# Optimization experiments

Hardware: AMD Instinct MI355X
Metric: run time of the kernel (lower is better)

## Reference

```python
import jax, jax.numpy as jnp
import numpy as np

N, B, CIN, HID, D, K = 2048, 16, 2, 64, 16, 2


def setup_inputs() -> dict:
    key = jax.random.key(0)
    ks = jax.random.split(key, 7)
    return {
        "X": jax.random.normal(ks[0], (B, N, CIN), dtype=jnp.float32),
        "state": jax.random.normal(ks[1], (B, N, HID), dtype=jnp.float32),
        "E": jax.random.normal(ks[2], (N, D), dtype=jnp.float32),
        "gate_W": jax.random.normal(ks[3], (D, K, CIN + HID, 2 * HID), dtype=jnp.float32) * 0.1,
        "gate_b": jax.random.normal(ks[4], (D, 2 * HID), dtype=jnp.float32) * 0.1,
        "upd_W": jax.random.normal(ks[5], (D, K, CIN + HID, HID), dtype=jnp.float32) * 0.1,
        "upd_b": jax.random.normal(ks[6], (D, HID), dtype=jnp.float32) * 0.1,
    }


def avwgcn(X, E, Wp, bp, k):
    # Adaptive adjacency: softmax(relu(E E^T)) over rows, [N,N]
    n = E.shape[0]
    supports = jax.nn.softmax(jax.nn.relu(E @ E.T), axis=1)
    support_set = [jnp.eye(n, dtype=supports.dtype), supports]
    for _ in range(2, k):  # Chebyshev recursion (no-op for K=2)
        support_set.append(2.0 * supports @ support_set[-1] - support_set[-2])
    S = jnp.stack(support_set, axis=0)                      # [K,N,N]
    W = jnp.einsum('nd,dkio->nkio', E, Wp)                  # per-node weights
    bias = E @ bp                                           # [N,Co]
    Xg = jnp.einsum('knm,bmc->bknc', S, X)                  # graph conv
    Xg = Xg.transpose(0, 2, 1, 3)                           # [B,N,K,Ci]
    return jnp.einsum('bnki,nkio->bno', Xg, W) + bias


def reference(X, state, E, gate_W, gate_b, upd_W, upd_b):
    input_and_state = jnp.concatenate((X, state), axis=-1)
    z_r = jax.nn.sigmoid(avwgcn(input_and_state, E, gate_W, gate_b, K))
    z, r = z_r[..., :HID], z_r[..., HID:]
    candidate = jnp.concatenate((X, z * state), axis=-1)
    hc = jnp.tanh(avwgcn(candidate, E, upd_W, upd_b, K))
    h = r * state + (1.0 - r) * hc
    return h
```

## Files before the change

### kernel.cpp

```cpp
#include <hip/hip_runtime.h>
#include <math.h>

#define NN   2048
#define BB   16
#define CINC 2
#define HID  64
#define C1   66
#define NC   1056
#define NCP  1152
#define KI   132
#define KIP  168

typedef unsigned short u16;
typedef __attribute__((ext_vector_type(8))) short bf16x8;
typedef __attribute__((ext_vector_type(4))) float f32x4;

__device__ __forceinline__ u16 f2bf(float f) {
    union { float f; unsigned int u; } v; v.f = f;
    unsigned int r = (v.u + 0x7FFFu + ((v.u >> 16) & 1u)) >> 16;
    return (u16)r;
}
__device__ __forceinline__ float bf2f(u16 h) {
    union { unsigned int u; float f; } v; v.u = ((unsigned int)h) << 16;
    return v.f;
}

__global__ __launch_bounds__(256) void support_softmax(const float* __restrict__ E,
                                                       u16* __restrict__ S)
{
    const int n = blockIdx.x, t = threadIdx.x;
    __shared__ float red[4];
    float en[16];
#pragma unroll
    for (int d = 0; d < 16; ++d) en[d] = E[n * 16 + d];

    float v[8]; float mx = 0.f;
#pragma unroll
    for (int j = 0; j < 8; ++j) {
        const int m = t + j * 256;
        const float4* ep = (const float4*)&E[m * 16];
        float4 e0 = ep[0], e1 = ep[1], e2 = ep[2], e3 = ep[3];
        float dot = en[0]*e0.x + en[1]*e0.y + en[2]*e0.z + en[3]*e0.w
                  + en[4]*e1.x + en[5]*e1.y + en[6]*e1.z + en[7]*e1.w
                  + en[8]*e2.x + en[9]*e2.y + en[10]*e2.z + en[11]*e2.w
                  + en[12]*e3.x + en[13]*e3.y + en[14]*e3.z + en[15]*e3.w;
        dot = fmaxf(dot, 0.f);
        v[j] = dot; mx = fmaxf(mx, dot);
    }
#pragma unroll
    for (int off = 32; off; off >>= 1) mx = fmaxf(mx, __shfl_down(mx, off, 64));
    const int wid = t >> 6, lane = t & 63;
    if (lane == 0) red[wid] = mx;
    __syncthreads();
    mx = fmaxf(fmaxf(red[0], red[1]), fmaxf(red[2], red[3]));

    float s = 0.f;
#pragma unroll
    for (int j = 0; j < 8; ++j) { v[j] = expf(v[j] - mx); s += v[j]; }
#pragma unroll
    for (int off = 32; off; off >>= 1) s += __shfl_down(s, off, 64);
    __syncthreads();
    if (lane == 0) red[wid] = s;
    __syncthreads();
    s = red[0] + red[1] + red[2] + red[3];
    const float inv = 1.f / s;
#pragma unroll
    for (int j = 0; j < 8; ++j) S[n * NN + t + j * 256] = f2bf(v[j] * inv);
}

__global__ __launch_bounds__(256) void build_xcatT(const float* __restrict__ X,
                                                   const float* __restrict__ state,
                                                   u16* __restrict__ XT)
{
    const int idx = blockIdx.x * 256 + threadIdx.x;
    const int m = idx & (NN - 1), j = idx >> 11;
    float val = 0.f;
    if (j < NC) {
        const int b = j / C1, c = j - b * C1;
        val = (c < CINC) ? X[(b * NN + m) * CINC + c]
                         : state[(b * NN + m) * HID + (c - CINC)];
    }
    XT[(size_t)j * NN + m] = f2bf(val);
}

template<int O>
__global__ __launch_bounds__(256) void bias_build(const float* __restrict__ E,
                                                  const float* __restrict__ bvec,
                                                  float* __restrict__ bias)
{
    const int idx = blockIdx.x * 256 + threadIdx.x;
    const int o = idx % O, n = idx / O;
    float s = 0.f;
#pragma unroll
    for (int d = 0; d < 16; ++d) s += E[n * 16 + d] * bvec[d * O + o];
    bias[idx] = s;
}

template<int O>
__global__ __launch_bounds__(256) void wbuild(const float* __restrict__ E,
                                              const float* __restrict__ Wp,
                                              u16* __restrict__ Wall)
{
    const int t = threadIdx.x;
    const int n0 = blockIdx.y * 16;
    __shared__ float El[256];
    El[t] = E[n0 * 16 + t];
    __syncthreads();

    const int nchunks = (KI * O) / 256;
    for (int ch = blockIdx.x; ch < nchunks; ch += gridDim.x) {
        const int flat = ch * 256 + t;
        float w[16];
#pragma unroll
        for (int d = 0; d < 16; ++d) w[d] = Wp[d * (KI * O) + flat];
#pragma unroll 4
        for (int g = 0; g < 16; ++g) {
            float s = 0.f;
#pragma unroll
            for (int d = 0; d < 16; ++d) s += El[g * 16 + d] * w[d];
            Wall[(size_t)(n0 + g) * (KI * O) + flat] = f2bf(s);
        }
    }
}

__global__ __launch_bounds__(256) void gemm64(const u16* __restrict__ A,
                                              const u16* __restrict__ BT,
                                              u16* __restrict__ C)
{
    __shared__ u16 As[64 * 32];
    __shared__ u16 Bs[64 * 32];
    const int t = threadIdx.x, w = t >> 6, l = t & 63;
    const int m0 = blockIdx.y * 64, n0 = blockIdx.x * 64;
    const int wm = (w >> 1) * 32, wn = (w & 1) * 32;

    const int srow = w * 16 + (l >> 2), scol = (l & 3) * 8;
    const size_t ga0 = (size_t)(m0 + srow) * NN + scol;
    const size_t gb0 = (size_t)(n0 + srow) * NN + scol;
    const int soff = srow * 32 + scol;

    f32x4 acc[2][2];
#pragma unroll
    for (int i = 0; i < 2; ++i)
#pragma unroll
        for (int j = 0; j < 2; ++j) acc[i][j] = f32x4{0.f, 0.f, 0.f, 0.f};

    for (int k0 = 0; k0 < NN; k0 += 32) {
        bf16x8 av = *(const bf16x8*)&A[ga0 + k0];
        bf16x8 bv = *(const bf16x8*)&BT[gb0 + k0];
        *(bf16x8*)&As[soff] = av;
        *(bf16x8*)&Bs[soff] = bv;
        __syncthreads();
        bf16x8 af[2], bfr[2];
#pragma unroll
        for (int mi = 0; mi < 2; ++mi)
            af[mi] = *(const bf16x8*)&As[(wm + mi * 16 + (l & 15)) * 32 + (l >> 4) * 8];
#pragma unroll
        for (int nj = 0; nj < 2; ++nj)
            bfr[nj] = *(const bf16x8*)&Bs[(wn + nj * 16 + (l & 15)) * 32 + (l >> 4) * 8];
#pragma unroll
        for (int mi = 0; mi < 2; ++mi)
#pragma unroll
            for (int nj = 0; nj < 2; ++nj)
                acc[mi][nj] = __builtin_amdgcn_mfma_f32_16x16x32_bf16(af[mi], bfr[nj], acc[mi][nj], 0, 0, 0);
        __syncthreads();
    }
#pragma unroll
    for (int mi = 0; mi < 2; ++mi)
#pragma unroll
        for (int nj = 0; nj < 2; ++nj)
#pragma unroll
            for (int q = 0; q < 4; ++q) {
                const int row = m0 + wm + mi * 16 + (l >> 4) * 4 + q;
                const int col = n0 + wn + nj * 16 + (l & 15);
                C[(size_t)row * NCP + col] = f2bf(acc[mi][nj][q]);
            }
}

__global__ __launch_bounds__(256) void apply_gate(const u16* __restrict__ Wg,
                                                  const float* __restrict__ biasg,
                                                  const float* __restrict__ X,
                                                  const float* __restrict__ state,
                                                  const u16* __restrict__ Zg,
                                                  u16* __restrict__ candRow,
                                                  float* __restrict__ rbuf)
{
    const int t = threadIdx.x, wv = t >> 6, l = t & 63;
    const int node = blockIdx.x * 4 + wv;
    __shared__ u16 Al[4][16 * KIP];
    u16* base = Al[wv];

    for (int i = l; i < 16 * KIP; i += 64) base[i] = 0;
    for (int f = l; f < 32; f += 64) {
        const int b = f >> 1, c = f & 1;
        base[b * KIP + c] = f2bf(X[(b * NN + node) * CINC + c]);
    }
#pragma unroll
    for (int k = 0; k < 16; ++k)
        base[k * KIP + 2 + l] = f2bf(state[(k * NN + node) * HID + l]);
    for (int f = l; f < NC; f += 64) {
        const int b = f / C1, i = f - b * C1;
        base[b * KIP + C1 + i] = Zg[(size_t)node * NCP + f];
    }
    __syncthreads();

    bf16x8 aF[5];
#pragma unroll
    for (int kc = 0; kc < 5; ++kc)
        aF[kc] = *(const bf16x8*)&base[(l & 15) * KIP + kc * 32 + (l >> 4) * 8];

    const u16* wp_n = Wg + (size_t)node * (KI * 128);
#pragma unroll 2
    for (int ct = 0; ct < 8; ++ct) {
        f32x4 acc = f32x4{0.f, 0.f, 0.f, 0.f};
#pragma unroll
        for (int kc = 0; kc < 5; ++kc) {
            const u16* wp = wp_n + (size_t)(kc * 32 + (l >> 4) * 8) * 128 + ct * 16 + (l & 15);
            bf16x8 bF;
#pragma unroll
            for (int j = 0; j < 8; ++j) bF[j] = (short)wp[j * 128];
            acc = __builtin_amdgcn_mfma_f32_16x16x32_bf16(aF[kc], bF, acc, 0, 0, 0);
        }
#pragma unroll
        for (int q = 0; q < 4; ++q) {
            const int b = (l >> 4) * 4 + q;
            const int o = ct * 16 + (l & 15);
            const float y = acc[q] + biasg[node * 128 + o];
            const float sg = 1.f / (1.f + expf(-y));
            if (o < 64) {
                candRow[(size_t)node * NCP + b * C1 + CINC + o] =
                    f2bf(sg * state[(b * NN + node) * HID + o]);
            } else {
                rbuf[((size_t)node * BB + b) * HID + (o - 64)] = sg;
            }
        }
    }
    for (int f = l; f < 32; f += 64) {
        const int b = f >> 1, c = f & 1;
        candRow[(size_t)node * NCP + b * C1 + c] = f2bf(X[(b * NN + node) * CINC + c]);
    }
}

__global__ __launch_bounds__(256) void transpose_pad(const u16* __restrict__ in,
                                                     u16* __restrict__ out)
{
    __shared__ u16 tile[64][65];
    const int t = threadIdx.x;
    const int j0 = blockIdx.x * 64, m0 = blockIdx.y * 64;
    for (int r = t >> 6; r < 64; r += 4)
        tile[r][t & 63] = in[(size_t)(m0 + r) * NCP + j0 + (t & 63)];
    __syncthreads();
    for (int r = t >> 6; r < 64; r += 4) {
        const int j = j0 + r;
        const u16 val = (j < NC) ? tile[t & 63][r] : (u16)0;
        out[(size_t)j * NN + m0 + (t & 63)] = val;
    }
}

__global__ __launch_bounds__(256) void apply_upd(const u16* __restrict__ Wu,
                                                 const float* __restrict__ biasu,
                                                 const u16* __restrict__ candRow,
                                                 const u16* __restrict__ Zu,
                                                 const float* __restrict__ state,
                                                 const float* __restrict__ rbuf,
                                                 float* __restrict__ out)
{
    const int t = threadIdx.x, wv = t >> 6, l = t & 63;
    const int node = blockIdx.x * 4 + wv;
    __shared__ u16 Al[4][16 * KIP];
    u16* base = Al[wv];

    for (int i = l; i < 16 * KIP; i += 64) base[i] = 0;
    for (int f = l; f < NC; f += 64) {
        const int b = f / C1, i = f - b * C1;
        base[b * KIP + i]      = candRow[(size_t)node * NCP + f];
        base[b * KIP + C1 + i] = Zu[(size_t)node * NCP + f];
    }
    __syncthreads();

    bf16x8 aF[5];
#pragma unroll
    for (int kc = 0; kc < 5; ++kc)
        aF[kc] = *(const bf16x8*)&base[(l & 15) * KIP + kc * 32 + (l >> 4) * 8];

    const u16* wp_n = Wu + (size_t)node * (KI * 64);
#pragma unroll 2
    for (int ct = 0; ct < 4; ++ct) {
        f32x4 acc = f32x4{0.f, 0.f, 0.f, 0.f};
#pragma unroll
        for (int kc = 0; kc < 5; ++kc) {
            const u16* wp = wp_n + (size_t)(kc * 32 + (l >> 4) * 8) * 64 + ct * 16 + (l & 15);
            bf16x8 bF;
#pragma unroll
            for (int j = 0; j < 8; ++j) bF[j] = (short)wp[j * 64];
            acc = __builtin_amdgcn_mfma_f32_16x16x32_bf16(aF[kc], bF, acc, 0, 0, 0);
        }
#pragma unroll
        for (int q = 0; q < 4; ++q) {
            const int b = (l >> 4) * 4 + q;
            const int o = ct * 16 + (l & 15);
            const float hc = tanhf(acc[q] + biasu[node * 64 + o]);
            const float r  = rbuf[((size_t)node * BB + b) * HID + o];
            const float st = state[(b * NN + node) * HID + o];
            out[(size_t)(b * NN + node) * HID + o] = r * st + (1.f - r) * hc;
        }
    }
}

extern "C" void kernel_launch(void* const* d_in, const int* in_sizes, int n_in,
                              void* d_out, int out_size, void* d_ws, size_t ws_size,
                              hipStream_t stream)
{
    const float* X     = (const float*)d_in[0];
    const float* state = (const float*)d_in[1];
    const float* E     = (const float*)d_in[2];
    const float* gW    = (const float*)d_in[3];
    const float* gb    = (const float*)d_in[4];
    const float* uW    = (const float*)d_in[5];
    const float* ub    = (const float*)d_in[6];
    float* out = (float*)d_out;

    char* ws = (char*)d_ws;
    u16*   S_bf   = (u16*)(ws);
    u16*   XcatT  = (u16*)(ws + 8388608);
    u16*   Zg     = (u16*)(ws + 13107200);
    u16*   candR  = (u16*)(ws + 17825792);
    u16*   candT  = (u16*)(ws + 22544384);
    u16*   Zu     = (u16*)(ws + 27262976);
    u16*   Wreg   = (u16*)(ws + 31981568);
    float* rbuf   = (float*)(ws + 101253120);
    float* biasg  = (float*)(ws + 109641728);
    float* biasu  = (float*)(ws + 110690304);

    support_softmax<<<NN, 256, 0, stream>>>(E, S_bf);
    build_xcatT<<<(NCP * NN) / 256, 256, 0, stream>>>(X, state, XcatT);
    bias_build<128><<<(NN * 128) / 256, 256, 0, stream>>>(E, gb, biasg);
    bias_build<64><<<(NN * 64) / 256, 256, 0, stream>>>(E, ub, biasu);
    wbuild<128><<<dim3(4, 128), 256, 0, stream>>>(E, gW, Wreg);
    gemm64<<<dim3(NCP / 64, NN / 64), 256, 0, stream>>>(S_bf, XcatT, Zg);
    apply_gate<<<NN / 4, 256, 0, stream>>>(Wreg, biasg, X, state, Zg, candR, rbuf);
    wbuild<64><<<dim3(4, 128), 256, 0, stream>>>(E, uW, Wreg);
    transpose_pad<<<dim3(NCP / 64, NN / 64), 256, 0, stream>>>(candR, candT);
    gemm64<<<dim3(NCP / 64, NN / 64), 256, 0, stream>>>(S_bf, candT, Zu);
    apply_upd<<<NN / 4, 256, 0, stream>>>(Wreg, biasu, candR, Zu, state, rbuf, out);
}
```

Baseline: 305.5 us.

## Pre-swizzle per-node weights into MFMA fragment layout, enlarge GEMM tile, fuse bias

Per-node weights are now written directly in the MFMA B-fragment order, so the apply kernels load one 16-byte vector per MFMA instead of eight strided scalar loads. The support GEMM moves to a 128x64 tile with register prefetch of the next K slice and padded LDS pitch to reduce bank conflicts. Bias computation is folded into the apply kernels, removing two launches. The r buffer is stored as bf16 and workspace buffers are aliased. The cost is extra register pressure in the GEMM and slightly lower precision for r.

```diff
diff --git a/kernel.cpp b/kernel.cpp
--- a/kernel.cpp
+++ b/kernel.cpp
@@ -10,6 +10,7 @@
 #define NCP  1152
 #define KI   132
 #define KIP  168
+#define KS   5
 
 typedef unsigned short u16;
 typedef __attribute__((ext_vector_type(8))) short bf16x8;
@@ -19,10 +20,6 @@
     union { float f; unsigned int u; } v; v.f = f;
     unsigned int r = (v.u + 0x7FFFu + ((v.u >> 16) & 1u)) >> 16;
     return (u16)r;
-}
-__device__ __forceinline__ float bf2f(u16 h) {
-    union { unsigned int u; float f; } v; v.u = ((unsigned int)h) << 16;
-    return v.f;
 }
 
 __global__ __launch_bounds__(256) void support_softmax(const float* __restrict__ E,
@@ -83,89 +80,105 @@
     XT[(size_t)j * NN + m] = f2bf(val);
 }
 
-template<int O>
-__global__ __launch_bounds__(256) void bias_build(const float* __restrict__ E,
-                                                  const float* __restrict__ bvec,
-                                                  float* __restrict__ bias)
-{
-    const int idx = blockIdx.x * 256 + threadIdx.x;
-    const int o = idx % O, n = idx / O;
-    float s = 0.f;
-#pragma unroll
-    for (int d = 0; d < 16; ++d) s += E[n * 16 + d] * bvec[d * O + o];
-    bias[idx] = s;
-}
-
-template<int O>
-__global__ __launch_bounds__(256) void wbuild(const float* __restrict__ E,
-                                              const float* __restrict__ Wp,
-                                              u16* __restrict__ Wall)
+template<int NCT>
+__global__ __launch_bounds__(256) void wbuild_sw(const float* __restrict__ E,
+                                                 const float* __restrict__ Wp,
+                                                 u16* __restrict__ Wsw)
 {
     const int t = threadIdx.x;
+    const int slot = blockIdx.x * 256 + t;
+    const int l = slot & 63, ks = (slot >> 6) % KS, ct = slot / (KS * 64);
     const int n0 = blockIdx.y * 16;
+    const int O = NCT * 16;
     __shared__ float El[256];
     El[t] = E[n0 * 16 + t];
     __syncthreads();
 
-    const int nchunks = (KI * O) / 256;
-    for (int ch = blockIdx.x; ch < nchunks; ch += gridDim.x) {
-        const int flat = ch * 256 + t;
-        float w[16];
-#pragma unroll
-        for (int d = 0; d < 16; ++d) w[d] = Wp[d * (KI * O) + flat];
-#pragma unroll 4
+    const int o = ct * 16 + (l & 15);
+    const int kibase = ks * 32 + (l >> 4) * 8;
+
+    uint4 pk[16];
+#pragma unroll
+    for (int jp = 0; jp < 4; ++jp) {
+        const int ki0 = kibase + 2 * jp, ki1 = ki0 + 1;
+        float w0[16], w1[16];
+#pragma unroll
+        for (int d = 0; d < 16; ++d) {
+            w0[d] = (ki0 < KI) ? Wp[d * (KI * O) + ki0 * O + o] : 0.f;
+            w1[d] = (ki1 < KI) ? Wp[d * (KI * O) + ki1 * O + o] : 0.f;
+        }
+#pragma unroll
         for (int g = 0; g < 16; ++g) {
-            float s = 0.f;
-#pragma unroll
-            for (int d = 0; d < 16; ++d) s += El[g * 16 + d] * w[d];
-            Wall[(size_t)(n0 + g) * (KI * O) + flat] = f2bf(s);
-        }
-    }
-}
-
-__global__ __launch_bounds__(256) void gemm64(const u16* __restrict__ A,
-                                              const u16* __restrict__ BT,
-                                              u16* __restrict__ C)
-{
-    __shared__ u16 As[64 * 32];
-    __shared__ u16 Bs[64 * 32];
+            float s0 = 0.f, s1 = 0.f;
+#pragma unroll
+            for (int d = 0; d < 16; ++d) {
+                const float e = El[g * 16 + d];
+                s0 += e * w0[d]; s1 += e * w1[d];
+            }
+            unsigned int packed = (unsigned int)f2bf(s0) | ((unsigned int)f2bf(s1) << 16);
+            ((unsigned int*)&pk[g])[jp] = packed;
+        }
+    }
+#pragma unroll
+    for (int g = 0; g < 16; ++g) {
+        const size_t base = ((((size_t)(n0 + g) * NCT + ct) * KS + ks) * 64 + l) * 8;
+        *(uint4*)&Wsw[base] = pk[g];
+    }
+}
+
+#define APITCH 40
+__global__ __launch_bounds__(256) void gemm_bt(const u16* __restrict__ A,
+                                               const u16* __restrict__ BT,
+                                               u16* __restrict__ C)
+{
+    __shared__ u16 As[128 * APITCH];
+    __shared__ u16 Bs[64 * APITCH];
     const int t = threadIdx.x, w = t >> 6, l = t & 63;
-    const int m0 = blockIdx.y * 64, n0 = blockIdx.x * 64;
-    const int wm = (w >> 1) * 32, wn = (w & 1) * 32;
-
-    const int srow = w * 16 + (l >> 2), scol = (l & 3) * 8;
-    const size_t ga0 = (size_t)(m0 + srow) * NN + scol;
-    const size_t gb0 = (size_t)(n0 + srow) * NN + scol;
-    const int soff = srow * 32 + scol;
-
-    f32x4 acc[2][2];
-#pragma unroll
-    for (int i = 0; i < 2; ++i)
+    const int m0 = blockIdx.y * 128, n0 = blockIdx.x * 64;
+    const int wm = (w >> 1) * 64, wn = (w & 1) * 32;
+
+    const int rA0 = t >> 2, rA1 = 64 + (t >> 2), qA = (t & 3) * 8;
+    const int rB  = t >> 2;
+    const size_t gA0 = (size_t)(m0 + rA0) * NN + qA;
+    const size_t gA1 = (size_t)(m0 + rA1) * NN + qA;
+    const size_t gB  = (size_t)(n0 + rB) * NN + qA;
+
+    f32x4 acc[4][2];
+#pragma unroll
+    for (int i = 0; i < 4; ++i)
 #pragma unroll
         for (int j = 0; j < 2; ++j) acc[i][j] = f32x4{0.f, 0.f, 0.f, 0.f};
 
+    bf16x8 va0 = *(const bf16x8*)&A[gA0];
+    bf16x8 va1 = *(const bf16x8*)&A[gA1];
+    bf16x8 vb  = *(const bf16x8*)&BT[gB];
+
     for (int k0 = 0; k0 < NN; k0 += 32) {
-        bf16x8 av = *(const bf16x8*)&A[ga0 + k0];
-        bf16x8 bv = *(const bf16x8*)&BT[gb0 + k0];
-        *(bf16x8*)&As[soff] = av;
-        *(bf16x8*)&Bs[soff] = bv;
+        *(bf16x8*)&As[rA0 * APITCH + qA] = va0;
+        *(bf16x8*)&As[rA1 * APITCH + qA] = va1;
+        *(bf16x8*)&Bs[rB  * APITCH + qA] = vb;
         __syncthreads();
-        bf16x8 af[2], bfr[2];
-#pragma unroll
-        for (int mi = 0; mi < 2; ++mi)
-            af[mi] = *(const bf16x8*)&As[(wm + mi * 16 + (l & 15)) * 32 + (l >> 4) * 8];
+        if (k0 + 32 < NN) {
+            va0 = *(const bf16x8*)&A[gA0 + k0 + 32];
+            va1 = *(const bf16x8*)&A[gA1 + k0 + 32];
+            vb  = *(const bf16x8*)&BT[gB + k0 + 32];
+        }
+        bf16x8 af[4], bfr[2];
+#pragma unroll
+        for (int mi = 0; mi < 4; ++mi)
+            af[mi] = *(const bf16x8*)&As[(wm + mi * 16 + (l & 15)) * APITCH + (l >> 4) * 8];
 #pragma unroll
         for (int nj = 0; nj < 2; ++nj)
-            bfr[nj] = *(const bf16x8*)&Bs[(wn + nj * 16 + (l & 15)) * 32 + (l >> 4) * 8];
-#pragma unroll
-        for (int mi = 0; mi < 2; ++mi)
+            bfr[nj] = *(const bf16x8*)&Bs[(wn + nj * 16 + (l & 15)) * APITCH + (l >> 4) * 8];
+#pragma unroll
+        for (int mi = 0; mi < 4; ++mi)
 #pragma unroll
             for (int nj = 0; nj < 2; ++nj)
                 acc[mi][nj] = __builtin_amdgcn_mfma_f32_16x16x32_bf16(af[mi], bfr[nj], acc[mi][nj], 0, 0, 0);
         __syncthreads();
     }
 #pragma unroll
-    for (int mi = 0; mi < 2; ++mi)
+    for (int mi = 0; mi < 4; ++mi)
 #pragma unroll
         for (int nj = 0; nj < 2; ++nj)
 #pragma unroll
@@ -177,17 +190,30 @@
 }
 
 __global__ __launch_bounds__(256) void apply_gate(const u16* __restrict__ Wg,
-                                                  const float* __restrict__ biasg,
+                                                  const float* __restrict__ E,
+                                                  const float* __restrict__ gb,
                                                   const float* __restrict__ X,
                                                   const float* __restrict__ state,
                                                   const u16* __restrict__ Zg,
                                                   u16* __restrict__ candRow,
-                                                  float* __restrict__ rbuf)
+                                                  u16* __restrict__ rbuf)
 {
     const int t = threadIdx.x, wv = t >> 6, l = t & 63;
     const int node = blockIdx.x * 4 + wv;
     __shared__ u16 Al[4][16 * KIP];
+    __shared__ float biasw[4][128];
     u16* base = Al[wv];
+
+    {
+        float b0 = 0.f, b1 = 0.f;
+#pragma unroll
+        for (int d = 0; d < 16; ++d) {
+            const float e = E[node * 16 + d];
+            b0 += e * gb[d * 128 + l];
+            b1 += e * gb[d * 128 + 64 + l];
+        }
+        biasw[wv][l] = b0; biasw[wv][l + 64] = b1;
+    }
 
     for (int i = l; i < 16 * KIP; i += 64) base[i] = 0;
     for (int f = l; f < 32; f += 64) {
@@ -203,34 +229,31 @@
     }
     __syncthreads();
 
-    bf16x8 aF[5];
-#pragma unroll
-    for (int kc = 0; kc < 5; ++kc)
+    bf16x8 aF[KS];
+#pragma unroll
+    for (int kc = 0; kc < KS; ++kc)
         aF[kc] = *(const bf16x8*)&base[(l & 15) * KIP + kc * 32 + (l >> 4) * 8];
 
-    const u16* wp_n = Wg + (size_t)node * (KI * 128);
+    const u16* wp_n = Wg + (((size_t)node * 8) * KS) * 512;
 #pragma unroll 2
     for (int ct = 0; ct < 8; ++ct) {
         f32x4 acc = f32x4{0.f, 0.f, 0.f, 0.f};
 #pragma unroll
-        for (int kc = 0; kc < 5; ++kc) {
-            const u16* wp = wp_n + (size_t)(kc * 32 + (l >> 4) * 8) * 128 + ct * 16 + (l & 15);
-            bf16x8 bF;
-#pragma unroll
-            for (int j = 0; j < 8; ++j) bF[j] = (short)wp[j * 128];
+        for (int kc = 0; kc < KS; ++kc) {
+            bf16x8 bF = *(const bf16x8*)&wp_n[(((size_t)ct * KS + kc) * 64 + l) * 8];
             acc = __builtin_amdgcn_mfma_f32_16x16x32_bf16(aF[kc], bF, acc, 0, 0, 0);
         }
 #pragma unroll
         for (int q = 0; q < 4; ++q) {
             const int b = (l >> 4) * 4 + q;
             const int o = ct * 16 + (l & 15);
-            const float y = acc[q] + biasg[node * 128 + o];
+            const float y = acc[q] + biasw[wv][o];
             const float sg = 1.f / (1.f + expf(-y));
             if (o < 64) {
                 candRow[(size_t)node * NCP + b * C1 + CINC + o] =
                     f2bf(sg * state[(b * NN + node) * HID + o]);
             } else {
-                rbuf[((size_t)node * BB + b) * HID + (o - 64)] = sg;
+                rbuf[((size_t)node * BB + b) * HID + (o - 64)] = f2bf(sg);
             }
         }
     }
@@ -257,17 +280,26 @@
 }
 
 __global__ __launch_bounds__(256) void apply_upd(const u16* __restrict__ Wu,
-                                                 const float* __restrict__ biasu,
+                                                 const float* __restrict__ E,
+                                                 const float* __restrict__ ub,
                                                  const u16* __restrict__ candRow,
                                                  const u16* __restrict__ Zu,
                                                  const float* __restrict__ state,
-                                                 const float* __restrict__ rbuf,
+                                                 const u16* __restrict__ rbuf,
                                                  float* __restrict__ out)
 {
     const int t = threadIdx.x, wv = t >> 6, l = t & 63;
     const int node = blockIdx.x * 4 + wv;
     __shared__ u16 Al[4][16 * KIP];
+    __shared__ float biasw[4][64];
     u16* base = Al[wv];
+
+    if (l < 64) {
+        float b0 = 0.f;
+#pragma unroll
+        for (int d = 0; d < 16; ++d) b0 += E[node * 16 + d] * ub[d * 64 + l];
+        biasw[wv][l] = b0;
+    }
 
     for (int i = l; i < 16 * KIP; i += 64) base[i] = 0;
     for (int f = l; f < NC; f += 64) {
@@ -277,29 +309,28 @@
     }
     __syncthreads();
 
-    bf16x8 aF[5];
-#pragma unroll
-    for (int kc = 0; kc < 5; ++kc)
+    bf16x8 aF[KS];
+#pragma unroll
+    for (int kc = 0; kc < KS; ++kc)
         aF[kc] = *(const bf16x8*)&base[(l & 15) * KIP + kc * 32 + (l >> 4) * 8];
 
-    const u16* wp_n = Wu + (size_t)node * (KI * 64);
+    const u16* wp_n = Wu + (((size_t)node * 4) * KS) * 512;
 #pragma unroll 2
     for (int ct = 0; ct < 4; ++ct) {
         f32x4 acc = f32x4{0.f, 0.f, 0.f, 0.f};
 #pragma unroll
-        for (int kc = 0; kc < 5; ++kc) {
-            const u16* wp = wp_n + (size_t)(kc * 32 + (l >> 4) * 8) * 64 + ct * 16 + (l & 15);
-            bf16x8 bF;
-#pragma unroll
-            for (int j = 0; j < 8; ++j) bF[j] = (short)wp[j * 64];
+        for (int kc = 0; kc < KS; ++kc) {
+            bf16x8 bF = *(const bf16x8*)&wp_n[(((size_t)ct * KS + kc) * 64 + l) * 8];
             acc = __builtin_amdgcn_mfma_f32_16x16x32_bf16(aF[kc], bF, acc, 0, 0, 0);
         }
 #pragma unroll
         for (int q = 0; q < 4; ++q) {
             const int b = (l >> 4) * 4 + q;
             const int o = ct * 16 + (l & 15);
-            const float hc = tanhf(acc[q] + biasu[node * 64 + o]);
-            const float r  = rbuf[((size_t)node * BB + b) * HID + o];
+            const float hc = tanhf(acc[q] + biasw[wv][o]);
+            union { unsigned int u; float f; } rv;
+            rv.u = ((unsigned int)rbuf[((size_t)node * BB + b) * HID + o]) << 16;
+            const float r = rv.f;
             const float st = state[(b * NN + node) * HID + o];
             out[(size_t)(b * NN + node) * HID + o] = r * st + (1.f - r) * hc;
         }
@@ -320,26 +351,22 @@
     float* out = (float*)d_out;
 
     char* ws = (char*)d_ws;
-    u16*   S_bf   = (u16*)(ws);
-    u16*   XcatT  = (u16*)(ws + 8388608);
-    u16*   Zg     = (u16*)(ws + 13107200);
-    u16*   candR  = (u16*)(ws + 17825792);
-    u16*   candT  = (u16*)(ws + 22544384);
-    u16*   Zu     = (u16*)(ws + 27262976);
-    u16*   Wreg   = (u16*)(ws + 31981568);
-    float* rbuf   = (float*)(ws + 101253120);
-    float* biasg  = (float*)(ws + 109641728);
-    float* biasu  = (float*)(ws + 110690304);
+    u16* S_bf  = (u16*)(ws);
+    u16* XcatT = (u16*)(ws + 8388608);
+    u16* Zg    = (u16*)(ws + 13107200);
+    u16* candR = (u16*)(ws + 17825792);
+    u16* rbuf  = (u16*)(ws + 22544384);
+    u16* Wsw   = (u16*)(ws + 26738688);
+    u16* candT = Zg;
+    u16* Zu    = XcatT;
 
     support_softmax<<<NN, 256, 0, stream>>>(E, S_bf);
     build_xcatT<<<(NCP * NN) / 256, 256, 0, stream>>>(X, state, XcatT);
-    bias_build<128><<<(NN * 128) / 256, 256, 0, stream>>>(E, gb, biasg);
-    bias_build<64><<<(NN * 64) / 256, 256, 0, stream>>>(E, ub, biasu);
-    wbuild<128><<<dim3(4, 128), 256, 0, stream>>>(E, gW, Wreg);
-    gemm64<<<dim3(NCP / 64, NN / 64), 256, 0, stream>>>(S_bf, XcatT, Zg);
-    apply_gate<<<NN / 4, 256, 0, stream>>>(Wreg, biasg, X, state, Zg, candR, rbuf);
-    wbuild<64><<<dim3(4, 128), 256, 0, stream>>>(E, uW, Wreg);
+    wbuild_sw<8><<<dim3(10, 128), 256, 0, stream>>>(E, gW, Wsw);
+    gemm_bt<<<dim3(NCP / 64, NN / 128), 256, 0, stream>>>(S_bf, XcatT, Zg);
+    apply_gate<<<NN / 4, 256, 0, stream>>>(Wsw, E, gb, X, state, Zg, candR, rbuf);
     transpose_pad<<<dim3(NCP / 64, NN / 64), 256, 0, stream>>>(candR, candT);
-    gemm64<<<dim3(NCP / 64, NN / 64), 256, 0, stream>>>(S_bf, candT, Zu);
-    apply_upd<<<NN / 4, 256, 0, stream>>>(Wreg, biasu, candR, Zu, state, rbuf, out);
-}
+    wbuild_sw<4><<<dim3(5, 128), 256, 0, stream>>>(E, uW, Wsw);
+    gemm_bt<<<dim3(NCP / 64, NN / 128), 256, 0, stream>>>(S_bf, candT, Zu);
+    apply_upd<<<NN / 4, 256, 0, stream>>>(Wsw, E, ub, candR, Zu, state, rbuf, out);
+}
```

After: 468.2 us. +53.3%, slower.
